# Kernel optimization log

Measured on AMD Instinct MI355X. Metric: run time of the kernel, lower is better.

## Reference

```python
import jax, jax.numpy as jnp
import numpy as np
from jax import lax

B = 1024          # batch_size
T = 20            # timesteps == input_timesteps
IN_DIM = 13       # data_in_dims
OUT_DIM = 9       # data_out_dims
SU = 32           # input_units == output_units (story / weight dim)
H = 32            # LowerRNN hidden_size
INFER_LR = 0.1
INFER_ITERS = 20
L2_LAMBDA = 1e-4
B1, B2, EPS = 0.9, 0.999, 1e-8  # torch.optim.Adam defaults


def _lin_init(key, fan_in, shape):
    bound = 1.0 / np.sqrt(fan_in)
    return jax.random.uniform(key, shape, jnp.float32, -bound, bound)


def setup_inputs() -> dict:
    key = jax.random.key(0)
    ks = jax.random.split(key, 20)
    return {
        "temporal_batch_input": jax.random.normal(ks[0], (T, B, IN_DIM), jnp.float32),
        "temporal_batch_output": jax.random.uniform(ks[1], (T, B, OUT_DIM), jnp.float32),
        # hypernet: 32 -> 128 -> 256 -> 256 -> 32 (ReLU between, linear out)
        "hW1": _lin_init(ks[2], SU, (SU, 128)),   "hb1": _lin_init(ks[3], SU, (128,)),
        "hW2": _lin_init(ks[4], 128, (128, 256)), "hb2": _lin_init(ks[5], 128, (256,)),
        "hW3": _lin_init(ks[6], 256, (256, 256)), "hb3": _lin_init(ks[7], 256, (256,)),
        "hW4": _lin_init(ks[8], 256, (256, SU)),  "hb4": _lin_init(ks[9], 256, (SU,)),
        # LowerRNN: tanh RNN, input 45 = cat(x:13, weights:32)
        "Wih": _lin_init(ks[10], H, (H, IN_DIM + SU)),
        "Whh": _lin_init(ks[11], H, (H, H)),
        "bih": _lin_init(ks[12], H, (H,)),
        "bhh": _lin_init(ks[13], H, (H,)),
        # decoder: Linear(32 -> 9), ReLU applied after
        "Wd": _lin_init(ks[14], H, (H, OUT_DIM)),
        "bd": _lin_init(ks[15], H, (OUT_DIM,)),
    }


def reference(temporal_batch_input, temporal_batch_output,
              hW1, hb1, hW2, hb2, hW3, hb3, hW4, hb4,
              Wih, Whh, bih, bhh, Wd, bd):
    def hyper(s):  # [B,32] -> [B,32]
        h = jax.nn.relu(s @ hW1 + hb1)
        h = jax.nn.relu(h @ hW2 + hb2)
        h = jax.nn.relu(h @ hW3 + hb3)
        return h @ hW4 + hb4

    def rnn_cell(x, h):  # torch nn.RNN tanh cell
        return jnp.tanh(x @ Wih.T + bih + h @ Whh.T + bhh)

    def infer_loss(story, x_t, y_t, hidden):
        w = hyper(story)
        h_new = rnn_cell(jnp.concatenate([x_t, w], axis=1), hidden)
        pred = jax.nn.relu(h_new @ Wd + bd)                       # [B,9]
        err = jnp.mean(jnp.sum((y_t - pred) ** 2, axis=-1))       # batch_errors
        loss = (err
                + jnp.sum(jnp.var(story, axis=0, ddof=1))         # torch.var unbiased
                + L2_LAMBDA * jnp.mean(jnp.sum(story ** 2, axis=-1)))
        return loss, h_new

    grad_fn = jax.grad(infer_loss, has_aux=True)

    def timestep(story, xy):
        # fresh Adam state + fresh hidden every outer timestep (new optimizer each call)
        x_t, y_t = xy
        def adam_iter(carry, i):
            s, m, v, h = carry
            g, h_new = grad_fn(s, x_t, y_t, h)   # hidden is detached in torch -> constant here
            t = (i + 1).astype(s.dtype)
            m = B1 * m + (1.0 - B1) * g
            v = B2 * v + (1.0 - B2) * g * g
            mhat = m / (1.0 - B1 ** t)
            vhat = v / (1.0 - B2 ** t)
            s = s - INFER_LR * mhat / (jnp.sqrt(vhat) + EPS)
            return (s, m, v, h_new), None
        z = jnp.zeros_like(story)
        h0 = jnp.zeros((story.shape[0], H), story.dtype)
        (story, _, _, _), _ = lax.scan(adam_iter, (story, z, z, h0), jnp.arange(INFER_ITERS))
        return story, None

    story0 = jnp.zeros((B, SU), jnp.float32)
    higher, _ = lax.scan(timestep, story0, (temporal_batch_input, temporal_batch_output))
    higher = lax.stop_gradient(higher)  # story is .clone().detach() in torch

    cluster_centers = jnp.mean(higher, axis=0)  # [32]
    w = hyper(higher)                           # [B,32], broadcast over T (repeat)

    def seq_step(h, x_t):
        h = rnn_cell(jnp.concatenate([x_t, w], axis=1), h)
        return h, h
    _, hs = lax.scan(seq_step, jnp.zeros((B, H), jnp.float32), temporal_batch_input)
    preds = jax.nn.relu(hs @ Wd + bd)           # [T,B,9]
    errors = jnp.mean(jnp.sum((preds - temporal_batch_output) ** 2, axis=(0, 2)))
    return errors, cluster_centers
```

## Files before the change

kernel.cpp:

```cpp
#include <hip/hip_runtime.h>

#define NB 256
#define NT 1024

constexpr int BATCH = 1024;
constexpr int TSTEPS = 20;
constexpr int IND = 13;
constexpr int OD = 9;
constexpr int SU = 32;
constexpr int HID = 32;
constexpr int ITERS = 20;
constexpr float LR = 0.1f;
constexpr float AB1 = 0.9f;
constexpr float AB2 = 0.999f;
constexpr float AEPS = 1e-8f;

constexpr unsigned SPIN_CAP = 1u << 27;

constexpr size_t OFF_CNT   = 0;
constexpr size_t OFF_ERRP  = 3072;
constexpr size_t OFF_PART  = 4096;
constexpr size_t OFF_WIHT  = 69632;
constexpr size_t OFF_WHHT  = 75392;
constexpr size_t OFF_W2T   = 79488;
constexpr size_t OFF_W3T   = 210560;
constexpr size_t OFF_W4T   = 472704;
constexpr size_t WS_NEEDED = 505472;

__device__ __forceinline__ float ld_coh_f32(const float* p) {
  return __hip_atomic_load(p, __ATOMIC_RELAXED, __HIP_MEMORY_SCOPE_AGENT);
}
__device__ __forceinline__ void st_coh_f32(float* p, float v) {
  __hip_atomic_store(p, v, __ATOMIC_RELAXED, __HIP_MEMORY_SCOPE_AGENT);
}

__device__ __forceinline__ void fma4(float4& a, const float4 w, const float h) {
  a.x += w.x * h; a.y += w.y * h; a.z += w.z * h; a.w += w.w * h;
}
__device__ __forceinline__ float dot4(const float4 a, const float4 b) {
  return a.x * b.x + a.y * b.y + a.z * b.z + a.w * b.w;
}

__global__ void prep_kernel(const float* __restrict__ Wih,
                            const float* __restrict__ Whh,
                            const float* __restrict__ W2,
                            const float* __restrict__ W3,
                            const float* __restrict__ W4,
                            char* __restrict__ ws) {
  float* WihT = reinterpret_cast<float*>(ws + OFF_WIHT);
  float* WhhT = reinterpret_cast<float*>(ws + OFF_WHHT);
  float* W2T  = reinterpret_cast<float*>(ws + OFF_W2T);
  float* W3T  = reinterpret_cast<float*>(ws + OFF_W3T);
  float* W4T  = reinterpret_cast<float*>(ws + OFF_W4T);
  int tid = blockIdx.x * blockDim.x + threadIdx.x;
  int nt = gridDim.x * blockDim.x;
  for (int idx = tid; idx < 32 * 45; idx += nt) {
    int i = idx / 45, c = idx % 45;
    WihT[c * 32 + i] = Wih[idx];
  }
  for (int idx = tid; idx < 32 * 32; idx += nt) {
    int i = idx >> 5, j = idx & 31;
    WhhT[j * 32 + i] = Whh[idx];
  }
  for (int idx = tid; idx < 256 * 128; idx += nt) {
    int k = idx >> 7, j = idx & 127;
    W2T[idx] = W2[j * 256 + k];
  }
  for (int idx = tid; idx < 256 * 256; idx += nt) {
    int k = idx >> 8, j = idx & 255;
    W3T[idx] = W3[j * 256 + k];
  }
  for (int idx = tid; idx < 32 * 256; idx += nt) {
    int k = idx >> 8, j = idx & 255;
    W4T[idx] = W4[j * 32 + k];
  }
}

__global__ __launch_bounds__(NT) void emb_kernel(
    const float* __restrict__ X, const float* __restrict__ Y,
    const float* __restrict__ pW1, const float* __restrict__ pb1,
    const float* __restrict__ pW2, const float* __restrict__ pb2,
    const float* __restrict__ pW3, const float* __restrict__ pb3,
    const float* __restrict__ pW4, const float* __restrict__ pb4,
    const float* __restrict__ pWih, const float* __restrict__ pWhh,
    const float* __restrict__ pbih, const float* __restrict__ pbhh,
    const float* __restrict__ pWd, const float* __restrict__ pbd,
    char* __restrict__ ws, float* __restrict__ out) {
  const int tid = threadIdx.x;
  const int bid = blockIdx.x;
  const int row0 = bid * 4;
  const int t  = tid & 511;
  const int rA = (tid >> 9) * 2, rB = rA + 1;

  unsigned* cnt = reinterpret_cast<unsigned*>(ws + OFF_CNT);
  float* errp = reinterpret_cast<float*>(ws + OFF_ERRP);
  float* part = reinterpret_cast<float*>(ws + OFF_PART);
  const float* WihT = reinterpret_cast<const float*>(ws + OFF_WIHT);
  const float* WhhT = reinterpret_cast<const float*>(ws + OFF_WHHT);
  const float* W2T  = reinterpret_cast<const float*>(ws + OFF_W2T);
  const float* W3T  = reinterpret_cast<const float*>(ws + OFF_W3T);
  const float* W4T  = reinterpret_cast<const float*>(ws + OFF_W4T);

  __shared__ alignas(16) float s[4][SU];
  __shared__ alignas(16) float mAd[4][SU];
  __shared__ alignas(16) float vAd[4][SU];
  __shared__ alignas(16) float hOld[4][HID];
  __shared__ alignas(16) float hNew[4][HID];
  __shared__ alignas(16) float h1[4][128];
  __shared__ alignas(16) float h2[4][256];
  __shared__ alignas(16) float h3[4][256];
  __shared__ alignas(16) float wv[4][SU];
  __shared__ alignas(16) float da[4][HID];
  __shared__ alignas(16) float dwb[4][SU];
  __shared__ alignas(16) float dsb[4][SU];
  __shared__ alignas(16) float red2[8192];
  __shared__ float xs[4][IND];
  __shared__ float ysd[4][OD];
  __shared__ float dadec[4][OD];
  __shared__ float red[32][SU];

  auto spin_ge = [&](unsigned* cntp, unsigned tgt) {
    unsigned n = 0;
    while (__hip_atomic_load(cntp, __ATOMIC_RELAXED,
                             __HIP_MEMORY_SCOPE_AGENT) < tgt) {
      __builtin_amdgcn_s_sleep(1);
      if (++n >= SPIN_CAP) break;
    }
  };


  auto fwd_l1 = [&]() {
    if (t < 256) {
      int j0 = (t & 31) * 4, kg = t >> 5;
      float4 aA = {0,0,0,0}, aB = aA;
#pragma unroll
      for (int q = 0; q < 4; ++q) {
        int k = kg * 4 + q;
        float4 w = *reinterpret_cast<const float4*>(pW1 + k * 128 + j0);
        fma4(aA, w, s[rA][k]); fma4(aB, w, s[rB][k]);
      }
      *reinterpret_cast<float4*>(&red2[(kg * 4 + rA) * 128 + j0]) = aA;
      *reinterpret_cast<float4*>(&red2[(kg * 4 + rB) * 128 + j0]) = aB;
    }
    __syncthreads();
    if (tid < 512) {
      int r = tid >> 7, j = tid & 127;
      float sum = pb1[j];
#pragma unroll
      for (int g = 0; g < 8; ++g) sum += red2[(g * 4 + r) * 128 + j];
      h1[r][j] = fmaxf(sum, 0.f);
    }
  };

  auto fwd_wide = [&](const float* __restrict__ W, const float* __restrict__ bias,
                      const float* hin, int K, float* hout) {
    {
      int j0 = (t & 63) * 4, kg = t >> 6;
      int kn = K >> 3;
      float4 aA = {0,0,0,0}, aB = aA;
#pragma unroll 8
      for (int q = 0; q < kn; ++q) {
        int k = kg * kn + q;
        float4 w = *reinterpret_cast<const float4*>(W + k * 256 + j0);
        fma4(aA, w, hin[rA * K + k]); fma4(aB, w, hin[rB * K + k]);
      }
      *reinterpret_cast<float4*>(&red2[(kg * 4 + rA) * 256 + j0]) = aA;
      *reinterpret_cast<float4*>(&red2[(kg * 4 + rB) * 256 + j0]) = aB;
    }
    __syncthreads();
    {
      int r = tid >> 8, j = tid & 255;
      float s0 = bias[j];
#pragma unroll
      for (int g = 0; g < 8; ++g) s0 += red2[(g * 4 + r) * 256 + j];
      hout[r * 256 + j] = fmaxf(s0, 0.f);
    }
  };

  auto fwd_l4 = [&]() {
    if (t < 128) {
      int j0 = (t & 7) * 4, kg = t >> 3;
      float4 aA = {0,0,0,0}, aB = aA;
#pragma unroll 8
      for (int q = 0; q < 16; ++q) {
        int k = kg * 16 + q;
        float4 w = *reinterpret_cast<const float4*>(pW4 + k * 32 + j0);
        fma4(aA, w, h3[rA][k]); fma4(aB, w, h3[rB][k]);
      }
      *reinterpret_cast<float4*>(&red2[(kg * 4 + rA) * 32 + j0]) = aA;
      *reinterpret_cast<float4*>(&red2[(kg * 4 + rB) * 32 + j0]) = aB;
    }
    __syncthreads();
    if (tid < 128) {
      int r = tid >> 5, j = tid & 31;
      float sum = pb4[j];
#pragma unroll
      for (int g = 0; g < 16; ++g) sum += red2[(g * 4 + r) * 32 + j];
      wv[r][j] = sum;
    }
  };

  auto rnn_fwd = [&]() {
    if (tid < 128) {
      int r = tid >> 5, i = tid & 31;
      float a = pbih[i] + pbhh[i];
#pragma unroll
      for (int c = 0; c < IND; ++c) a += xs[r][c] * WihT[c * 32 + i];
#pragma unroll 8
      for (int c = 0; c < SU; ++c) a += wv[r][c] * WihT[(13 + c) * 32 + i];
#pragma unroll 8
      for (int j = 0; j < HID; ++j) a += hOld[r][j] * WhhT[j * 32 + i];
      hNew[r][i] = tanhf(a);
    }
  };

  auto bwdT256 = [&](const float* __restrict__ WT, const float* din, int Kd,
                     float* dmask) {
    {
      int j0 = (t & 63) * 4, kg = t >> 6;
      int kn = Kd >> 3;
      float4 aA = {0,0,0,0}, aB = aA;
#pragma unroll 4
      for (int q = 0; q < kn; ++q) {
        int k = kg * kn + q;
        float4 w = *reinterpret_cast<const float4*>(WT + k * 256 + j0);
        fma4(aA, w, din[rA * Kd + k]); fma4(aB, w, din[rB * Kd + k]);
      }
      *reinterpret_cast<float4*>(&red2[(kg * 4 + rA) * 256 + j0]) = aA;
      *reinterpret_cast<float4*>(&red2[(kg * 4 + rB) * 256 + j0]) = aB;
    }
    __syncthreads();
    {
      int r = tid >> 8, j = tid & 255;
      float s0 = 0.f;
#pragma unroll
      for (int g = 0; g < 8; ++g) s0 += red2[(g * 4 + r) * 256 + j];
      float m0 = dmask[r * 256 + j];
      dmask[r * 256 + j] = (m0 > 0.f) ? s0 : 0.f;
    }
  };

  auto bwd_dh1 = [&]() {
    {
      int j0 = (t & 31) * 4, kg = t >> 5;
      float4 aA = {0,0,0,0}, aB = aA;
#pragma unroll 8
      for (int q = 0; q < 16; ++q) {
        int k = kg * 16 + q;
        float4 w = *reinterpret_cast<const float4*>(W2T + k * 128 + j0);
        fma4(aA, w, h2[rA][k]); fma4(aB, w, h2[rB][k]);
      }
      *reinterpret_cast<float4*>(&red2[(kg * 4 + rA) * 128 + j0]) = aA;
      *reinterpret_cast<float4*>(&red2[(kg * 4 + rB) * 128 + j0]) = aB;
    }
    __syncthreads();
    if (tid < 512) {
      int r = tid >> 7, j = tid & 127;
      float sum = 0.f;
#pragma unroll
      for (int g = 0; g < 16; ++g) sum += red2[(g * 4 + r) * 128 + j];
      h1[r][j] = (h1[r][j] > 0.f) ? sum : 0.f;
    }
  };

  auto bwd_ds = [&]() {
    if (t < 256) {
      int k0 = (t & 7) * 4, jg = t >> 3;
      int j0 = jg * 4;
      float4 gA = *reinterpret_cast<const float4*>(&h1[rA][j0]);
      float4 gB = *reinterpret_cast<const float4*>(&h1[rB][j0]);
      float4 aA, aB;
      float* A = &aA.x; float* Bp = &aB.x;
#pragma unroll
      for (int q = 0; q < 4; ++q) {
        int k = k0 + q;
        float4 w = *reinterpret_cast<const float4*>(pW1 + k * 128 + j0);
        A[q] = dot4(w, gA); Bp[q] = dot4(w, gB);
      }
      *reinterpret_cast<float4*>(&red2[jg * 128 + rA * 32 + k0]) = aA;
      *reinterpret_cast<float4*>(&red2[jg * 128 + rB * 32 + k0]) = aB;
    }
    __syncthreads();
    if (tid < 128) {
      int r = tid >> 5, k = tid & 31;
      float sum = 0.f;
#pragma unroll
      for (int g = 0; g < 32; ++g) sum += red2[g * 128 + r * 32 + k];
      dsb[r][k] = sum;
    }
  };

  auto publish = [&](int pslot) {
    __syncthreads();
    if (tid < SU) {
      st_coh_f32(&part[(size_t)pslot * NB * SU + (size_t)bid * SU + tid],
                 s[0][tid] + s[1][tid] + s[2][tid] + s[3][tid]);
    }
    if (tid == 0)
      __hip_atomic_fetch_add(&cnt[pslot], 1u, __ATOMIC_RELEASE,
                             __HIP_MEMORY_SCOPE_AGENT);
  };

  if (tid < 128) { int r = tid >> 5, c = tid & 31; s[r][c] = 0.f; }
  publish(0);

  for (int ts = 0; ts < TSTEPS; ++ts) {
    if (tid < 4 * IND) {
      int r = tid / IND, c = tid % IND;
      xs[r][c] = X[(size_t)ts * BATCH * IND + (size_t)(row0 + r) * IND + c];
    }
    if (tid >= 64 && tid < 64 + 4 * OD) {
      int q = tid - 64; int r = q / OD, c = q % OD;
      ysd[r][c] = Y[(size_t)ts * BATCH * OD + (size_t)(row0 + r) * OD + c];
    }
    if (tid >= 128 && tid < 256) {
      int q = tid - 128; int r = q >> 5, c = q & 31;
      mAd[r][c] = 0.f; vAd[r][c] = 0.f; hOld[r][c] = 0.f;
    }
    float pb1t = 1.f, pb2t = 1.f;

    for (int it = 0; it < ITERS; ++it) {
      const int gi = ts * ITERS + it;
      const int p = gi & 1;
      pb1t *= AB1; pb2t *= AB2;

      fwd_l1(); __syncthreads();
      fwd_wide(pW2, pb2, &h1[0][0], 128, &h2[0][0]); __syncthreads();
      fwd_wide(pW3, pb3, &h2[0][0], 256, &h3[0][0]); __syncthreads();
      fwd_l4(); __syncthreads();
      rnn_fwd(); __syncthreads();

      if (tid < 36) {
        int r = tid / OD, d = tid % OD;
        float adec = pbd[d];
#pragma unroll
        for (int i = 0; i < HID; ++i) adec += hNew[r][i] * pWd[i * OD + d];
        float pr = fmaxf(adec, 0.f);
        dadec[r][d] = (adec > 0.f) ? (2.f / 1024.f) * (pr - ysd[r][d]) : 0.f;
      }
      __syncthreads();

      if (tid < 128) {
        int r = tid >> 5, i = tid & 31;
        float t1 = 0.f;
#pragma unroll
        for (int d = 0; d < OD; ++d) t1 += dadec[r][d] * pWd[i * OD + d];
        float hn = hNew[r][i];
        da[r][i] = t1 * (1.f - hn * hn);
      }
      __syncthreads();

      if (tid < 128) {
        int r = tid >> 5, k = tid & 31;
        float t2 = 0.f;
#pragma unroll 8
        for (int i = 0; i < HID; ++i) t2 += da[r][i] * WihT[(13 + k) * 32 + i];
        dwb[r][k] = t2;
      }
      __syncthreads();

      bwdT256(W4T, &dwb[0][0], 32, &h3[0][0]); __syncthreads();
      bwdT256(W3T, &h3[0][0], 256, &h2[0][0]); __syncthreads();
      bwd_dh1(); __syncthreads();
      bwd_ds(); __syncthreads();

      if (tid == 0) spin_ge(&cnt[p], (unsigned)(gi / 2 + 1) * (unsigned)NB);
      __syncthreads();

      {
        int c = tid & 31, grp = tid >> 5;
        const float* P = part + (size_t)p * NB * SU;
        float sum = 0.f;
#pragma unroll
        for (int b2 = grp * 8; b2 < grp * 8 + 8; ++b2)
          sum += ld_coh_f32(&P[b2 * SU + c]);
        red[grp][c] = sum;
      }
      __syncthreads();

      if (tid < 128) {
        int r = tid >> 5, c = tid & 31;
        float msum = 0.f;
#pragma unroll
        for (int g = 0; g < 32; ++g) msum += red[g][c];
        float muc = msum * (1.f / 1024.f);
        float sv = s[r][c];
        float g = dsb[r][c] + (sv - muc) * (2.f / 1023.f) + sv * (2e-4f / 1024.f);
        float m2 = AB1 * mAd[r][c] + (1.f - AB1) * g;
        float v2 = AB2 * vAd[r][c] + (1.f - AB2) * g * g;
        mAd[r][c] = m2; vAd[r][c] = v2;
        float mh = m2 / (1.f - pb1t);
        float vh = v2 / (1.f - pb2t);
        s[r][c] = sv - LR * mh / (sqrtf(vh) + AEPS);
        hOld[r][c] = hNew[r][c];
      }

      publish((gi + 1) & 1);
    }
  }

  fwd_l1(); __syncthreads();
  fwd_wide(pW2, pb2, &h1[0][0], 128, &h2[0][0]); __syncthreads();
  fwd_wide(pW3, pb3, &h2[0][0], 256, &h3[0][0]); __syncthreads();
  fwd_l4(); __syncthreads();

  if (tid < 128) { int r = tid >> 5, i = tid & 31; hOld[r][i] = 0.f; }
  __syncthreads();

  float errACC = 0.f;
  for (int t2 = 0; t2 < TSTEPS; ++t2) {
    if (tid < 4 * IND) {
      int r = tid / IND, c = tid % IND;
      xs[r][c] = X[(size_t)t2 * BATCH * IND + (size_t)(row0 + r) * IND + c];
    }
    __syncthreads();
    rnn_fwd(); __syncthreads();
    if (tid < 36) {
      int r = tid / OD, d = tid % OD;
      float adec = pbd[d];
#pragma unroll
      for (int i = 0; i < HID; ++i) adec += hNew[r][i] * pWd[i * OD + d];
      float pr = fmaxf(adec, 0.f);
      float e = pr - Y[(size_t)t2 * BATCH * OD + (size_t)(row0 + r) * OD + d];
      errACC += e * e;
    }
    if (tid < 128) { int r = tid >> 5, i = tid & 31; hOld[r][i] = hNew[r][i]; }
    __syncthreads();
  }

  if (tid < 36) (&red[0][0])[tid] = errACC;
  __syncthreads();
  if (tid == 0) {
    float sum = 0.f;
    for (int q = 0; q < 36; ++q) sum += (&red[0][0])[q];
    st_coh_f32(&errp[bid], sum);
    __hip_atomic_fetch_add(&cnt[2], 1u, __ATOMIC_RELEASE,
                           __HIP_MEMORY_SCOPE_AGENT);
  }

  if (bid == 0) {
    if (tid == 0) {
      spin_ge(&cnt[2], (unsigned)NB);
      spin_ge(&cnt[0], (unsigned)(TSTEPS * ITERS / 2 + 1) * (unsigned)NB);
    }
    __syncthreads();
    if (tid == 0) {
      float sum = 0.f;
      for (int b = 0; b < NB; ++b) sum += ld_coh_f32(&errp[b]);
      out[0] = sum * (1.f / 1024.f);
    }
    if (tid >= 64 && tid < 96) {
      int c = tid - 64;
      float sum = 0.f;
      for (int b = 0; b < NB; ++b)
        sum += ld_coh_f32(&part[(size_t)b * SU + c]);
      out[1 + c] = sum * (1.f / 1024.f);
    }
  }
}

extern "C" void kernel_launch(void* const* d_in, const int* in_sizes, int n_in,
                              void* d_out, int out_size, void* d_ws, size_t ws_size,
                              hipStream_t stream) {
  (void)in_sizes; (void)n_in; (void)out_size;
  if (ws_size < WS_NEEDED) return;

  const float* X   = (const float*)d_in[0];
  const float* Y   = (const float*)d_in[1];
  const float* W1  = (const float*)d_in[2];
  const float* b1  = (const float*)d_in[3];
  const float* W2  = (const float*)d_in[4];
  const float* b2  = (const float*)d_in[5];
  const float* W3  = (const float*)d_in[6];
  const float* b3  = (const float*)d_in[7];
  const float* W4  = (const float*)d_in[8];
  const float* b4  = (const float*)d_in[9];
  const float* Wih = (const float*)d_in[10];
  const float* Whh = (const float*)d_in[11];
  const float* bih = (const float*)d_in[12];
  const float* bhh = (const float*)d_in[13];
  const float* Wd  = (const float*)d_in[14];
  const float* bd  = (const float*)d_in[15];

  hipMemsetAsync(d_ws, 0, 3072, stream);
  prep_kernel<<<128, 256, 0, stream>>>(Wih, Whh, W2, W3, W4, (char*)d_ws);
  emb_kernel<<<NB, NT, 0, stream>>>(X, Y, W1, b1, W2, b2, W3, b3, W4, b4,
                                    Wih, Whh, bih, bhh, Wd, bd,
                                    (char*)d_ws, (float*)d_out);
}
```

Measured before the change: 13.26 ms.

## Halve rows per block and double grid to 512 persistent blocks

Reassigns work so each block owns two batch rows instead of four, doubling the grid to 512 blocks. Each matvec stage now splits the reduction dimension across all 1024 threads, giving shorter per-thread loops and deeper shared-memory reductions. The intent is to cut per-block serial latency on each of the 400 inner iterations by spreading work over more CUs. The cost is doubled redundant weight reads, twice as many partial-sum publishers in the grid-wide mean reduction, and the requirement that all 512 blocks stay co-resident for the spin barrier.

```diff
diff --git a/kernel.cpp b/kernel.cpp
--- a/kernel.cpp
+++ b/kernel.cpp
@@ -1,6 +1,6 @@
 #include <hip/hip_runtime.h>
 
-#define NB 256
+#define NB 512
 #define NT 1024
 
 constexpr int BATCH = 1024;
@@ -19,13 +19,13 @@
 
 constexpr size_t OFF_CNT   = 0;
 constexpr size_t OFF_ERRP  = 3072;
-constexpr size_t OFF_PART  = 4096;
-constexpr size_t OFF_WIHT  = 69632;
-constexpr size_t OFF_WHHT  = 75392;
-constexpr size_t OFF_W2T   = 79488;
-constexpr size_t OFF_W3T   = 210560;
-constexpr size_t OFF_W4T   = 472704;
-constexpr size_t WS_NEEDED = 505472;
+constexpr size_t OFF_PART  = 5120;
+constexpr size_t OFF_WIHT  = 136192;
+constexpr size_t OFF_WHHT  = 141952;
+constexpr size_t OFF_W2T   = 146048;
+constexpr size_t OFF_W3T   = 277120;
+constexpr size_t OFF_W4T   = 539264;
+constexpr size_t WS_NEEDED = 572032;
 
 __device__ __forceinline__ float ld_coh_f32(const float* p) {
   return __hip_atomic_load(p, __ATOMIC_RELAXED, __HIP_MEMORY_SCOPE_AGENT);
@@ -76,7 +76,7 @@
   }
 }
 
-__global__ __launch_bounds__(NT) void emb_kernel(
+__global__ __launch_bounds__(NT, 8) void emb_kernel(
     const float* __restrict__ X, const float* __restrict__ Y,
     const float* __restrict__ pW1, const float* __restrict__ pb1,
     const float* __restrict__ pW2, const float* __restrict__ pb2,
@@ -88,9 +88,7 @@
     char* __restrict__ ws, float* __restrict__ out) {
   const int tid = threadIdx.x;
   const int bid = blockIdx.x;
-  const int row0 = bid * 4;
-  const int t  = tid & 511;
-  const int rA = (tid >> 9) * 2, rB = rA + 1;
+  const int row0 = bid * 2;
 
   unsigned* cnt = reinterpret_cast<unsigned*>(ws + OFF_CNT);
   float* errp = reinterpret_cast<float*>(ws + OFF_ERRP);
@@ -101,22 +99,22 @@
   const float* W3T  = reinterpret_cast<const float*>(ws + OFF_W3T);
   const float* W4T  = reinterpret_cast<const float*>(ws + OFF_W4T);
 
-  __shared__ alignas(16) float s[4][SU];
-  __shared__ alignas(16) float mAd[4][SU];
-  __shared__ alignas(16) float vAd[4][SU];
-  __shared__ alignas(16) float hOld[4][HID];
-  __shared__ alignas(16) float hNew[4][HID];
-  __shared__ alignas(16) float h1[4][128];
-  __shared__ alignas(16) float h2[4][256];
-  __shared__ alignas(16) float h3[4][256];
-  __shared__ alignas(16) float wv[4][SU];
-  __shared__ alignas(16) float da[4][HID];
-  __shared__ alignas(16) float dwb[4][SU];
-  __shared__ alignas(16) float dsb[4][SU];
+  __shared__ alignas(16) float s[2][SU];
+  __shared__ alignas(16) float mAd[2][SU];
+  __shared__ alignas(16) float vAd[2][SU];
+  __shared__ alignas(16) float hOld[2][HID];
+  __shared__ alignas(16) float hNew[2][HID];
+  __shared__ alignas(16) float h1[2][128];
+  __shared__ alignas(16) float h2[2][256];
+  __shared__ alignas(16) float h3[2][256];
+  __shared__ alignas(16) float wv[2][SU];
+  __shared__ alignas(16) float da[2][HID];
+  __shared__ alignas(16) float dwb[2][SU];
+  __shared__ alignas(16) float dsb[2][SU];
   __shared__ alignas(16) float red2[8192];
-  __shared__ float xs[4][IND];
-  __shared__ float ysd[4][OD];
-  __shared__ float dadec[4][OD];
+  __shared__ float xs[2][IND];
+  __shared__ float ysd[2][OD];
+  __shared__ float dadec[2][OD];
   __shared__ float red[32][SU];
 
   auto spin_ge = [&](unsigned* cntp, unsigned tgt) {
@@ -130,24 +128,20 @@
 
 
   auto fwd_l1 = [&]() {
-    if (t < 256) {
-      int j0 = (t & 31) * 4, kg = t >> 5;
-      float4 aA = {0,0,0,0}, aB = aA;
-#pragma unroll
-      for (int q = 0; q < 4; ++q) {
-        int k = kg * 4 + q;
-        float4 w = *reinterpret_cast<const float4*>(pW1 + k * 128 + j0);
-        fma4(aA, w, s[rA][k]); fma4(aB, w, s[rB][k]);
-      }
-      *reinterpret_cast<float4*>(&red2[(kg * 4 + rA) * 128 + j0]) = aA;
-      *reinterpret_cast<float4*>(&red2[(kg * 4 + rB) * 128 + j0]) = aB;
-    }
-    __syncthreads();
-    if (tid < 512) {
+    {
+      int j0 = (tid & 31) * 4, k = tid >> 5;
+      float4 a0 = {0, 0, 0, 0}, a1 = a0;
+      float4 w = *reinterpret_cast<const float4*>(pW1 + k * 128 + j0);
+      fma4(a0, w, s[0][k]); fma4(a1, w, s[1][k]);
+      *reinterpret_cast<float4*>(&red2[(k * 2 + 0) * 128 + j0]) = a0;
+      *reinterpret_cast<float4*>(&red2[(k * 2 + 1) * 128 + j0]) = a1;
+    }
+    __syncthreads();
+    if (tid < 256) {
       int r = tid >> 7, j = tid & 127;
       float sum = pb1[j];
-#pragma unroll
-      for (int g = 0; g < 8; ++g) sum += red2[(g * 4 + r) * 128 + j];
+#pragma unroll 8
+      for (int g = 0; g < 32; ++g) sum += red2[(g * 2 + r) * 128 + j];
       h1[r][j] = fmaxf(sum, 0.f);
     }
   };
@@ -155,53 +149,53 @@
   auto fwd_wide = [&](const float* __restrict__ W, const float* __restrict__ bias,
                       const float* hin, int K, float* hout) {
     {
-      int j0 = (t & 63) * 4, kg = t >> 6;
-      int kn = K >> 3;
-      float4 aA = {0,0,0,0}, aB = aA;
+      int j0 = (tid & 63) * 4, kg = tid >> 6;
+      int kn = K >> 4;
+      float4 a0 = {0, 0, 0, 0}, a1 = a0;
 #pragma unroll 8
       for (int q = 0; q < kn; ++q) {
         int k = kg * kn + q;
         float4 w = *reinterpret_cast<const float4*>(W + k * 256 + j0);
-        fma4(aA, w, hin[rA * K + k]); fma4(aB, w, hin[rB * K + k]);
-      }
-      *reinterpret_cast<float4*>(&red2[(kg * 4 + rA) * 256 + j0]) = aA;
-      *reinterpret_cast<float4*>(&red2[(kg * 4 + rB) * 256 + j0]) = aB;
-    }
-    __syncthreads();
-    {
+        fma4(a0, w, hin[k]); fma4(a1, w, hin[K + k]);
+      }
+      *reinterpret_cast<float4*>(&red2[(kg * 2 + 0) * 256 + j0]) = a0;
+      *reinterpret_cast<float4*>(&red2[(kg * 2 + 1) * 256 + j0]) = a1;
+    }
+    __syncthreads();
+    if (tid < 512) {
       int r = tid >> 8, j = tid & 255;
       float s0 = bias[j];
 #pragma unroll
-      for (int g = 0; g < 8; ++g) s0 += red2[(g * 4 + r) * 256 + j];
+      for (int g = 0; g < 16; ++g) s0 += red2[(g * 2 + r) * 256 + j];
       hout[r * 256 + j] = fmaxf(s0, 0.f);
     }
   };
 
   auto fwd_l4 = [&]() {
-    if (t < 128) {
-      int j0 = (t & 7) * 4, kg = t >> 3;
-      float4 aA = {0,0,0,0}, aB = aA;
-#pragma unroll 8
-      for (int q = 0; q < 16; ++q) {
-        int k = kg * 16 + q;
+    if (tid < 256) {
+      int j0 = (tid & 7) * 4, kg = tid >> 3;
+      float4 a0 = {0, 0, 0, 0}, a1 = a0;
+#pragma unroll
+      for (int q = 0; q < 8; ++q) {
+        int k = kg * 8 + q;
         float4 w = *reinterpret_cast<const float4*>(pW4 + k * 32 + j0);
-        fma4(aA, w, h3[rA][k]); fma4(aB, w, h3[rB][k]);
-      }
-      *reinterpret_cast<float4*>(&red2[(kg * 4 + rA) * 32 + j0]) = aA;
-      *reinterpret_cast<float4*>(&red2[(kg * 4 + rB) * 32 + j0]) = aB;
-    }
-    __syncthreads();
-    if (tid < 128) {
+        fma4(a0, w, h3[0][k]); fma4(a1, w, h3[1][k]);
+      }
+      *reinterpret_cast<float4*>(&red2[(kg * 2 + 0) * 32 + j0]) = a0;
+      *reinterpret_cast<float4*>(&red2[(kg * 2 + 1) * 32 + j0]) = a1;
+    }
+    __syncthreads();
+    if (tid < 64) {
       int r = tid >> 5, j = tid & 31;
       float sum = pb4[j];
-#pragma unroll
-      for (int g = 0; g < 16; ++g) sum += red2[(g * 4 + r) * 32 + j];
+#pragma unroll 8
+      for (int g = 0; g < 32; ++g) sum += red2[(g * 2 + r) * 32 + j];
       wv[r][j] = sum;
     }
   };
 
   auto rnn_fwd = [&]() {
-    if (tid < 128) {
+    if (tid < 64) {
       int r = tid >> 5, i = tid & 31;
       float a = pbih[i] + pbhh[i];
 #pragma unroll
@@ -217,24 +211,24 @@
   auto bwdT256 = [&](const float* __restrict__ WT, const float* din, int Kd,
                      float* dmask) {
     {
-      int j0 = (t & 63) * 4, kg = t >> 6;
-      int kn = Kd >> 3;
-      float4 aA = {0,0,0,0}, aB = aA;
-#pragma unroll 4
+      int j0 = (tid & 63) * 4, kg = tid >> 6;
+      int kn = Kd >> 4;
+      float4 a0 = {0, 0, 0, 0}, a1 = a0;
+#pragma unroll 8
       for (int q = 0; q < kn; ++q) {
         int k = kg * kn + q;
         float4 w = *reinterpret_cast<const float4*>(WT + k * 256 + j0);
-        fma4(aA, w, din[rA * Kd + k]); fma4(aB, w, din[rB * Kd + k]);
-      }
-      *reinterpret_cast<float4*>(&red2[(kg * 4 + rA) * 256 + j0]) = aA;
-      *reinterpret_cast<float4*>(&red2[(kg * 4 + rB) * 256 + j0]) = aB;
-    }
-    __syncthreads();
-    {
+        fma4(a0, w, din[k]); fma4(a1, w, din[Kd + k]);
+      }
+      *reinterpret_cast<float4*>(&red2[(kg * 2 + 0) * 256 + j0]) = a0;
+      *reinterpret_cast<float4*>(&red2[(kg * 2 + 1) * 256 + j0]) = a1;
+    }
+    __syncthreads();
+    if (tid < 512) {
       int r = tid >> 8, j = tid & 255;
       float s0 = 0.f;
 #pragma unroll
-      for (int g = 0; g < 8; ++g) s0 += red2[(g * 4 + r) * 256 + j];
+      for (int g = 0; g < 16; ++g) s0 += red2[(g * 2 + r) * 256 + j];
       float m0 = dmask[r * 256 + j];
       dmask[r * 256 + j] = (m0 > 0.f) ? s0 : 0.f;
     }
@@ -242,33 +236,33 @@
 
   auto bwd_dh1 = [&]() {
     {
-      int j0 = (t & 31) * 4, kg = t >> 5;
-      float4 aA = {0,0,0,0}, aB = aA;
-#pragma unroll 8
-      for (int q = 0; q < 16; ++q) {
-        int k = kg * 16 + q;
+      int j0 = (tid & 31) * 4, kg = tid >> 5;
+      float4 a0 = {0, 0, 0, 0}, a1 = a0;
+#pragma unroll
+      for (int q = 0; q < 8; ++q) {
+        int k = kg * 8 + q;
         float4 w = *reinterpret_cast<const float4*>(W2T + k * 128 + j0);
-        fma4(aA, w, h2[rA][k]); fma4(aB, w, h2[rB][k]);
-      }
-      *reinterpret_cast<float4*>(&red2[(kg * 4 + rA) * 128 + j0]) = aA;
-      *reinterpret_cast<float4*>(&red2[(kg * 4 + rB) * 128 + j0]) = aB;
-    }
-    __syncthreads();
-    if (tid < 512) {
+        fma4(a0, w, h2[0][k]); fma4(a1, w, h2[1][k]);
+      }
+      *reinterpret_cast<float4*>(&red2[(kg * 2 + 0) * 128 + j0]) = a0;
+      *reinterpret_cast<float4*>(&red2[(kg * 2 + 1) * 128 + j0]) = a1;
+    }
+    __syncthreads();
+    if (tid < 256) {
       int r = tid >> 7, j = tid & 127;
       float sum = 0.f;
-#pragma unroll
-      for (int g = 0; g < 16; ++g) sum += red2[(g * 4 + r) * 128 + j];
+#pragma unroll 8
+      for (int g = 0; g < 32; ++g) sum += red2[(g * 2 + r) * 128 + j];
       h1[r][j] = (h1[r][j] > 0.f) ? sum : 0.f;
     }
   };
 
   auto bwd_ds = [&]() {
-    if (t < 256) {
-      int k0 = (t & 7) * 4, jg = t >> 3;
+    if (tid < 256) {
+      int k0 = (tid & 7) * 4, jg = tid >> 3;
       int j0 = jg * 4;
-      float4 gA = *reinterpret_cast<const float4*>(&h1[rA][j0]);
-      float4 gB = *reinterpret_cast<const float4*>(&h1[rB][j0]);
+      float4 gA = *reinterpret_cast<const float4*>(&h1[0][j0]);
+      float4 gB = *reinterpret_cast<const float4*>(&h1[1][j0]);
       float4 aA, aB;
       float* A = &aA.x; float* Bp = &aB.x;
 #pragma unroll
@@ -277,15 +271,15 @@
         float4 w = *reinterpret_cast<const float4*>(pW1 + k * 128 + j0);
         A[q] = dot4(w, gA); Bp[q] = dot4(w, gB);
       }
-      *reinterpret_cast<float4*>(&red2[jg * 128 + rA * 32 + k0]) = aA;
-      *reinterpret_cast<float4*>(&red2[jg * 128 + rB * 32 + k0]) = aB;
-    }
-    __syncthreads();
-    if (tid < 128) {
+      *reinterpret_cast<float4*>(&red2[jg * 64 + 0 * 32 + k0]) = aA;
+      *reinterpret_cast<float4*>(&red2[jg * 64 + 1 * 32 + k0]) = aB;
+    }
+    __syncthreads();
+    if (tid < 64) {
       int r = tid >> 5, k = tid & 31;
       float sum = 0.f;
-#pragma unroll
-      for (int g = 0; g < 32; ++g) sum += red2[g * 128 + r * 32 + k];
+#pragma unroll 8
+      for (int g = 0; g < 32; ++g) sum += red2[g * 64 + r * 32 + k];
       dsb[r][k] = sum;
     }
   };
@@ -294,26 +288,26 @@
     __syncthreads();
     if (tid < SU) {
       st_coh_f32(&part[(size_t)pslot * NB * SU + (size_t)bid * SU + tid],
-                 s[0][tid] + s[1][tid] + s[2][tid] + s[3][tid]);
+                 s[0][tid] + s[1][tid]);
     }
     if (tid == 0)
       __hip_atomic_fetch_add(&cnt[pslot], 1u, __ATOMIC_RELEASE,
                              __HIP_MEMORY_SCOPE_AGENT);
   };
 
-  if (tid < 128) { int r = tid >> 5, c = tid & 31; s[r][c] = 0.f; }
+  if (tid < 64) { int r = tid >> 5, c = tid & 31; s[r][c] = 0.f; }
   publish(0);
 
   for (int ts = 0; ts < TSTEPS; ++ts) {
-    if (tid < 4 * IND) {
+    if (tid < 2 * IND) {
       int r = tid / IND, c = tid % IND;
       xs[r][c] = X[(size_t)ts * BATCH * IND + (size_t)(row0 + r) * IND + c];
     }
-    if (tid >= 64 && tid < 64 + 4 * OD) {
+    if (tid >= 64 && tid < 64 + 2 * OD) {
       int q = tid - 64; int r = q / OD, c = q % OD;
       ysd[r][c] = Y[(size_t)ts * BATCH * OD + (size_t)(row0 + r) * OD + c];
     }
-    if (tid >= 128 && tid < 256) {
+    if (tid >= 128 && tid < 192) {
       int q = tid - 128; int r = q >> 5, c = q & 31;
       mAd[r][c] = 0.f; vAd[r][c] = 0.f; hOld[r][c] = 0.f;
     }
@@ -330,7 +324,7 @@
       fwd_l4(); __syncthreads();
       rnn_fwd(); __syncthreads();
 
-      if (tid < 36) {
+      if (tid < 2 * OD) {
         int r = tid / OD, d = tid % OD;
         float adec = pbd[d];
 #pragma unroll
@@ -340,7 +334,7 @@
       }
       __syncthreads();
 
-      if (tid < 128) {
+      if (tid < 64) {
         int r = tid >> 5, i = tid & 31;
         float t1 = 0.f;
 #pragma unroll
@@ -350,7 +344,7 @@
       }
       __syncthreads();
 
-      if (tid < 128) {
+      if (tid < 64) {
         int r = tid >> 5, k = tid & 31;
         float t2 = 0.f;
 #pragma unroll 8
@@ -372,16 +366,16 @@
         const float* P = part + (size_t)p * NB * SU;
         float sum = 0.f;
 #pragma unroll
-        for (int b2 = grp * 8; b2 < grp * 8 + 8; ++b2)
+        for (int b2 = grp * 16; b2 < grp * 16 + 16; ++b2)
           sum += ld_coh_f32(&P[b2 * SU + c]);
         red[grp][c] = sum;
       }
       __syncthreads();
 
-      if (tid < 128) {
+      if (tid < 64) {
         int r = tid >> 5, c = tid & 31;
         float msum = 0.f;
-#pragma unroll
+#pragma unroll 8
         for (int g = 0; g < 32; ++g) msum += red[g][c];
         float muc = msum * (1.f / 1024.f);
         float sv = s[r][c];
@@ -404,18 +398,18 @@
   fwd_wide(pW3, pb3, &h2[0][0], 256, &h3[0][0]); __syncthreads();
   fwd_l4(); __syncthreads();
 
-  if (tid < 128) { int r = tid >> 5, i = tid & 31; hOld[r][i] = 0.f; }
+  if (tid < 64) { int r = tid >> 5, i = tid & 31; hOld[r][i] = 0.f; }
   __syncthreads();
 
   float errACC = 0.f;
   for (int t2 = 0; t2 < TSTEPS; ++t2) {
-    if (tid < 4 * IND) {
+    if (tid < 2 * IND) {
       int r = tid / IND, c = tid % IND;
       xs[r][c] = X[(size_t)t2 * BATCH * IND + (size_t)(row0 + r) * IND + c];
     }
     __syncthreads();
     rnn_fwd(); __syncthreads();
-    if (tid < 36) {
+    if (tid < 2 * OD) {
       int r = tid / OD, d = tid % OD;
       float adec = pbd[d];
 #pragma unroll
@@ -424,15 +418,15 @@
       float e = pr - Y[(size_t)t2 * BATCH * OD + (size_t)(row0 + r) * OD + d];
       errACC += e * e;
     }
-    if (tid < 128) { int r = tid >> 5, i = tid & 31; hOld[r][i] = hNew[r][i]; }
-    __syncthreads();
-  }
-
-  if (tid < 36) (&red[0][0])[tid] = errACC;
+    if (tid < 64) { int r = tid >> 5, i = tid & 31; hOld[r][i] = hNew[r][i]; }
+    __syncthreads();
+  }
+
+  if (tid < 2 * OD) (&red[0][0])[tid] = errACC;
   __syncthreads();
   if (tid == 0) {
     float sum = 0.f;
-    for (int q = 0; q < 36; ++q) sum += (&red[0][0])[q];
+    for (int q = 0; q < 2 * OD; ++q) sum += (&red[0][0])[q];
     st_coh_f32(&errp[bid], sum);
     __hip_atomic_fetch_add(&cnt[2], 1u, __ATOMIC_RELEASE,
                            __HIP_MEMORY_SCOPE_AGENT);
```

Result: slower. 33.06 ms (+149.2%).
